# Optimization experiments

Measured on AMD Instinct MI355X. Metric: run time of the kernel, lower is better.

The kernel has to match this reference:

```python
import jax, jax.numpy as jnp
import numpy as np

N, B, L, E = 64, 128, 4096, 16
BN_EPS = 1e-5


def setup_inputs() -> dict:
    key = jax.random.key(0)
    ks = jax.random.split(key, 6)
    feat = jax.random.normal(ks[0], (N, B, L), dtype=jnp.float32)
    # Glorot-ish scaled linear weights
    Wl = jax.random.normal(ks[1], (L, E), dtype=jnp.float32) * (1.0 / np.sqrt(L))
    Wr = jax.random.normal(ks[2], (L, E), dtype=jnp.float32) * (1.0 / np.sqrt(L))
    Wm = jax.random.normal(ks[3], (L, L), dtype=jnp.float32) * (1.0 / np.sqrt(L))
    return {
        "feat": feat,
        "Wl": Wl, "bl": jnp.zeros((E,), jnp.float32),
        "Wr": Wr, "br": jnp.zeros((E,), jnp.float32),
        "Wm": Wm, "bm": jnp.zeros((L,), jnp.float32),
        "gamma": jnp.ones((N * N,), jnp.float32),
        "beta": jnp.zeros((N * N,), jnp.float32),
        "bias": jnp.zeros((L,), jnp.float32),
    }


def reference(feat, Wl, bl, Wr, br, Wm, bm, gamma, beta, bias):
    # feat: (N, B, L) node time series
    # Attention projections (lookup_l / lookup_r): Linear(L -> E)
    att_l = feat @ Wl + bl                      # (N, B, E) on src nodes
    att_r = feat @ Wr + br                      # (N, B, E) on dst nodes

    # Feature extractor: MLP Linear(L, L) + ReLU over the time axis
    out = jax.nn.relu(jnp.einsum('nbl,kl->nbk', feat, Wm) + bm)   # (N, B, L)

    # Edge scores on the complete graph: e[d, s, b] = att_l[src=s] . att_r[dst=d]
    e = jnp.einsum('sbe,dbe->dsb', att_l, att_r)                  # (Nd, Ns, B)

    # BatchNorm1d over N*N edge channels (training-mode batch statistics)
    ef = e.reshape(N * N, B)
    mu = ef.mean(axis=1, keepdims=True)
    var = ef.var(axis=1, keepdims=True)
    ef = gamma[:, None] * (ef - mu) * jax.lax.rsqrt(var + BN_EPS) + beta[:, None]
    e = ef.reshape(N, N, B)

    # edge_softmax: normalize over incoming edges (src axis) per destination node
    w = jax.nn.softmax(e, axis=1)                                  # (Nd, Ns, B)

    # Weighted neighbor aggregation + bias
    rst = jnp.einsum('dsb,sbl->dbl', w, out) + bias                # (N, B, L)
    return rst
```

## Files before the change

### kernel.cpp

```cpp
#include <hip/hip_runtime.h>
#include <stdint.h>
#include <stddef.h>

#define NN 64
#define BB 128
#define LL 4096
#define EE 16

typedef __attribute__((ext_vector_type(4))) float f32x4;
typedef __attribute__((ext_vector_type(2))) float f32x2;
typedef __attribute__((ext_vector_type(8))) short short8;
typedef __attribute__((ext_vector_type(4))) unsigned short u16x4;

__device__ __forceinline__ unsigned short f2bf(float f) {
  union { float f; unsigned u; } v; v.f = f;
  unsigned r = v.u + 0x7FFFu + ((v.u >> 16) & 1u);
  return (unsigned short)(r >> 16);
}
__device__ __forceinline__ float bf2f(unsigned short h) {
  union { unsigned u; float f; } v; v.u = ((unsigned)h) << 16;
  return v.f;
}
__device__ __forceinline__ void gload16(const void* g, void* l) {
  __builtin_amdgcn_global_load_lds((const __attribute__((address_space(1))) void*)g,
                                   (__attribute__((address_space(3))) void*)l,
                                   16, 0, 0);
}

__global__ __launch_bounds__(256) void k_cvt(const float* __restrict__ src,
                                             unsigned short* __restrict__ dst, int n4) {
  int i = blockIdx.x * 256 + threadIdx.x;
  int stride = gridDim.x * 256;
  for (; i < n4; i += stride) {
    f32x4 v = ((const f32x4*)src)[i];
    u16x4 o;
    o[0] = f2bf(v[0]); o[1] = f2bf(v[1]); o[2] = f2bf(v[2]); o[3] = f2bf(v[3]);
    ((u16x4*)dst)[i] = o;
  }
}

__global__ __launch_bounds__(256) void k_att(const float* __restrict__ feat,
    const float* __restrict__ Wl, const float* __restrict__ bl,
    const float* __restrict__ Wr, const float* __restrict__ br,
    unsigned short* __restrict__ feat_bf,
    float* __restrict__ att_l, float* __restrict__ att_r) {
  __shared__ __align__(16) float wlds[128][36];
  __shared__ __align__(16) float flds[8][132];
  __shared__ __align__(16) float red[4][64][4];
  int t = threadIdx.x;
  int rowBase = blockIdx.x * 8;
  int lane = t & 63, wave = t >> 6;
  int row = lane >> 3, eg = lane & 7;
  float acc0 = 0.f, acc1 = 0.f, acc2 = 0.f, acc3 = 0.f;
  for (int kc = 0; kc < 32; ++kc) {
    int k0 = kc * 128;
    __syncthreads();
    for (int i = t; i < 512; i += 256) {
      int kk = i >> 2, ee = (i & 3) * 4;
      *(f32x4*)&wlds[kk][ee]      = *(const f32x4*)&Wl[(size_t)(k0 + kk) * 16 + ee];
      *(f32x4*)&wlds[kk][16 + ee] = *(const f32x4*)&Wr[(size_t)(k0 + kk) * 16 + ee];
    }
    {
      int rr = t >> 5, kk = (t & 31) * 4;
      size_t gi = (size_t)(rowBase + rr) * LL + k0 + kk;
      f32x4 v = *(const f32x4*)&feat[gi];
      *(f32x4*)&flds[rr][kk] = v;
      u16x4 o; o[0] = f2bf(v[0]); o[1] = f2bf(v[1]); o[2] = f2bf(v[2]); o[3] = f2bf(v[3]);
      *(u16x4*)&feat_bf[gi] = o;
    }
    __syncthreads();
    int kb = wave * 32;
    #pragma unroll
    for (int k2 = 0; k2 < 32; ++k2) {
      int k = kb + k2;
      float fv = flds[row][k];
      f32x4 wv = *(const f32x4*)&wlds[k][eg * 4];
      acc0 += fv * wv[0]; acc1 += fv * wv[1]; acc2 += fv * wv[2]; acc3 += fv * wv[3];
    }
  }
  red[wave][lane][0] = acc0; red[wave][lane][1] = acc1;
  red[wave][lane][2] = acc2; red[wave][lane][3] = acc3;
  __syncthreads();
  if (t < 64) {
    f32x4 s = *(f32x4*)&red[0][t][0];
    #pragma unroll
    for (int w2 = 1; w2 < 4; ++w2) {
      f32x4 v = *(f32x4*)&red[w2][t][0];
      s[0] += v[0]; s[1] += v[1]; s[2] += v[2]; s[3] += v[3];
    }
    int r = rowBase + (t >> 3);
    int e0 = (t & 7) * 4;
    #pragma unroll
    for (int q = 0; q < 4; ++q) {
      int e = e0 + q;
      if (e < 16) att_l[(size_t)r * 16 + e]        = s[q] + bl[e];
      else        att_r[(size_t)r * 16 + (e - 16)] = s[q] + br[e - 16];
    }
  }
}

__global__ __launch_bounds__(256) void k_edge(const float* __restrict__ att_l,
    const float* __restrict__ att_r, const float* __restrict__ gamma,
    const float* __restrict__ beta, float* __restrict__ w_t) {
  __shared__ __align__(16) float attr[BB][20];
  __shared__ float el[NN][BB + 1];
  __shared__ float part[NN][4][2];
  __shared__ float sc[NN], sh[NN];
  int d = blockIdx.x, t = threadIdx.x;
  for (int i = t; i < 512; i += 256) {
    int b = i >> 2, e = (i & 3) * 4;
    *(f32x4*)&attr[b][e] = *(const f32x4*)&att_r[((size_t)d * BB + b) * 16 + e];
  }
  __syncthreads();
  for (int v = t; v < NN * BB; v += 256) {
    int s = v >> 7, b = v & 127;
    const float* al = &att_l[((size_t)s * BB + b) * 16];
    float acc = 0.f;
    #pragma unroll
    for (int e4 = 0; e4 < 4; ++e4) {
      f32x4 a = *(const f32x4*)&al[e4 * 4];
      f32x4 r = *(const f32x4*)&attr[b][e4 * 4];
      acc += a[0] * r[0] + a[1] * r[1] + a[2] * r[2] + a[3] * r[3];
    }
    el[s][b] = acc;
  }
  __syncthreads();
  {
    int s = t >> 2, q = t & 3;
    float sum = 0.f, ss = 0.f;
    for (int b = q * 32; b < q * 32 + 32; ++b) { float x = el[s][b]; sum += x; ss += x * x; }
    part[s][q][0] = sum; part[s][q][1] = ss;
  }
  __syncthreads();
  if (t < 64) {
    float sum = 0.f, ss = 0.f;
    #pragma unroll
    for (int q = 0; q < 4; ++q) { sum += part[t][q][0]; ss += part[t][q][1]; }
    float mu = sum * (1.f / 128.f);
    float var = ss * (1.f / 128.f) - mu * mu;
    int c = d * 64 + t;
    float a = gamma[c] * rsqrtf(fmaxf(var, 0.f) + 1e-5f);
    sc[t] = a; sh[t] = beta[c] - mu * a;
  }
  __syncthreads();
  if (t < 128) {
    int b = t;
    float y[64];
    float m = -1e30f;
    #pragma unroll
    for (int s = 0; s < 64; ++s) { y[s] = sc[s] * el[s][b] + sh[s]; m = fmaxf(m, y[s]); }
    float sum = 0.f;
    #pragma unroll
    for (int s = 0; s < 64; ++s) { y[s] = __expf(y[s] - m); sum += y[s]; }
    float inv = 1.f / sum;
    float* wp = &w_t[((size_t)b * 64 + d) * 64];
    #pragma unroll
    for (int s4 = 0; s4 < 16; ++s4) {
      f32x4 o;
      o[0] = y[s4 * 4 + 0] * inv; o[1] = y[s4 * 4 + 1] * inv;
      o[2] = y[s4 * 4 + 2] * inv; o[3] = y[s4 * 4 + 3] * inv;
      *(f32x4*)&wp[s4 * 4] = o;
    }
  }
}

#define LDS_A 0
#define LDS_B 65536
#define BAR   __builtin_amdgcn_s_barrier()
#define LGKM0 asm volatile("s_waitcnt lgkmcnt(0)" ::: "memory")
#define LGKM8 asm volatile("s_waitcnt lgkmcnt(8)" ::: "memory")
#define VM6   asm volatile("s_waitcnt vmcnt(6)" ::: "memory")
#define VM4   asm volatile("s_waitcnt vmcnt(4)" ::: "memory")
#define VM0   asm volatile("s_waitcnt vmcnt(0)" ::: "memory")
#define PRIO1 __builtin_amdgcn_s_setprio(1)
#define PRIO0 __builtin_amdgcn_s_setprio(0)
#define MFMA(a, b, c) __builtin_amdgcn_mfma_f32_16x16x32_bf16((a), (b), (c), 0, 0, 0)
#define STAGE2(g0, g1, ldsoff) do { \
    gload16((g0), lds_raw + (ldsoff) + tid16); \
    gload16((g1), lds_raw + (ldsoff) + 8192 + tid16); } while (0)

__global__ __launch_bounds__(512, 2) void k_gemm8(const unsigned short* __restrict__ A,
    const unsigned short* __restrict__ Bm, const float* __restrict__ bm,
    unsigned short* __restrict__ C) {
  __shared__ __align__(16) char lds_raw[131072];
  const int tid = threadIdx.x;
  const int lane = tid & 63, wave = tid >> 6;
  const int wm = wave >> 2, wn = wave & 3;
  int bid = blockIdx.x;
  int swz = (bid & 7) * 64 + (bid >> 3);
  int tM = swz >> 4, tN = swz & 15;
  const size_t rowBase = (size_t)tM * 256, colBase = (size_t)tN * 256;
  const int tid16 = tid * 16;
  const int o0 = tid16, o1 = tid16 + 8192;
  const int r0s = (o0 & 1023) >> 6, r1s = (o1 & 1023) >> 6;
  const int row0 = (o0 >> 10) * 16 + r0s, row1 = (o1 >> 10) * 16 + r1s;
  const int col0 = (((o0 >> 4) & 3) ^ ((r0s >> 3) << 1)) * 8;
  const int col1 = (((o1 >> 4) & 3) ^ ((r1s >> 3) << 1)) * 8;
  const unsigned short* aR0 = A  + (rowBase + row0) * LL + col0;
  const unsigned short* aR1 = A  + (rowBase + row1) * LL + col1;
  const unsigned short* bR0 = Bm + (colBase + row0) * LL + col0;
  const unsigned short* bR1 = Bm + (colBase + row1) * LL + col1;
  const int rr = lane & 15, gg = lane >> 4;
  const int rdswz = rr * 64 + ((gg ^ ((rr >> 3) << 1)) << 4);
  f32x4 acc[8][4] = {};
  STAGE2(aR0 +  0, aR1 +  0, LDS_A + 0);
  STAGE2(bR0 +  0, bR1 +  0, LDS_B + 0);
  STAGE2(aR0 + 32, aR1 + 32, LDS_A + 16384);
  STAGE2(bR0 + 32, bR1 + 32, LDS_B + 16384);
  VM4;
  STAGE2(aR0 + 64, aR1 + 64, LDS_A + 32768);
  STAGE2(bR0 + 64, bR1 + 64, LDS_B + 32768);
  STAGE2(aR0 + 96, aR1 + 96, LDS_A + 32768 + 16384);
  VM6;
  BAR;
  #pragma unroll 2
  for (int t = 0; t < 64; ++t) {
    const int d = t & 1;
    const char* pA = lds_raw + LDS_A + d * 32768 + wm * 8192 + rdswz;
    const char* pB = lds_raw + LDS_B + d * 32768 + wn * 4096 + rdswz;
    short8 ar[8], bx, by;
    #pragma unroll
    for (int mi = 0; mi < 8; ++mi) ar[mi] = *(const short8*)(pA + mi * 1024);
    bx = *(const short8*)(pB + 0);
    by = *(const short8*)(pB + 1024);
    if (t <= 62) { size_t kc = (size_t)(t + 1) * 64 + 32;
      STAGE2(bR0 + kc, bR1 + kc, LDS_B + ((t + 1) & 1) * 32768 + 16384); }
    LGKM8;
    BAR; LGKM0; PRIO1;
    #pragma unroll
    for (int mi = 0; mi < 8; ++mi) {
      acc[mi][0] = MFMA(ar[mi], bx, acc[mi][0]);
      acc[mi][1] = MFMA(ar[mi], by, acc[mi][1]);
    }
    PRIO0; BAR;
    bx = *(const short8*)(pB + 2048);
    by = *(const short8*)(pB + 3072);
    if (t <= 61) { size_t kc = (size_t)(t + 2) * 64;
      STAGE2(aR0 + kc, aR1 + kc, LDS_A + d * 32768); }
    BAR; LGKM0; PRIO1;
    #pragma unroll
    for (int mi = 0; mi < 8; ++mi) {
      acc[mi][2] = MFMA(ar[mi], bx, acc[mi][2]);
      acc[mi][3] = MFMA(ar[mi], by, acc[mi][3]);
    }
    PRIO0; BAR;
    #pragma unroll
    for (int mi = 0; mi < 8; ++mi) ar[mi] = *(const short8*)(pA + 16384 + mi * 1024);
    bx = *(const short8*)(pB + 16384 + 2048);
    by = *(const short8*)(pB + 16384 + 3072);
    if (t <= 61) { size_t kc = (size_t)(t + 2) * 64;
      STAGE2(bR0 + kc, bR1 + kc, LDS_B + d * 32768); }
    LGKM8;
    BAR; LGKM0; PRIO1;
    #pragma unroll
    for (int mi = 0; mi < 8; ++mi) {
      acc[mi][2] = MFMA(ar[mi], bx, acc[mi][2]);
      acc[mi][3] = MFMA(ar[mi], by, acc[mi][3]);
    }
    PRIO0; BAR;
    bx = *(const short8*)(pB + 16384);
    by = *(const short8*)(pB + 16384 + 1024);
    if (t <= 61) { size_t kc = (size_t)(t + 2) * 64 + 32;
      STAGE2(aR0 + kc, aR1 + kc, LDS_A + d * 32768 + 16384); }
    BAR; LGKM0; PRIO1;
    #pragma unroll
    for (int mi = 0; mi < 8; ++mi) {
      acc[mi][0] = MFMA(ar[mi], bx, acc[mi][0]);
      acc[mi][1] = MFMA(ar[mi], by, acc[mi][1]);
    }
    PRIO0;
    if (t < 62) { VM6; } else { VM0; }
    BAR;
  }
  const int co = lane & 15, ro4 = (lane >> 4) * 4;
  #pragma unroll
  for (int mig = 0; mig < 8; ++mig) {
    size_t r0 = rowBase + (size_t)wm * 128 + mig * 16 + ro4;
    #pragma unroll
    for (int nj = 0; nj < 4; ++nj) {
      size_t c = colBase + (size_t)wn * 64 + nj * 16 + co;
      float bc = bm[c];
      #pragma unroll
      for (int j = 0; j < 4; ++j) {
        float v = acc[mig][nj][j] + bc;
        v = fmaxf(v, 0.f);
        C[(r0 + j) * LL + c] = f2bf(v);
      }
    }
  }
}

__global__ __launch_bounds__(256) void k_agg2(const float* __restrict__ w_t,
    const unsigned short* __restrict__ outb, const float* __restrict__ bias,
    float* __restrict__ rst) {
  int b = blockIdx.y;
  int t = threadIdx.x;
  int l0 = blockIdx.x * 512 + t * 2;
  float oA[64], oB[64];
  #pragma unroll
  for (int s = 0; s < 64; ++s) {
    unsigned u = *(const unsigned*)&outb[((size_t)s * BB + b) * LL + l0];
    oA[s] = bf2f((unsigned short)(u & 0xFFFF));
    oB[s] = bf2f((unsigned short)(u >> 16));
  }
  const float* wb = w_t + (size_t)b * 4096;
  float bs0 = bias[l0], bs1 = bias[l0 + 1];
  #pragma unroll 2
  for (int d = 0; d < 64; ++d) {
    const float* wr = wb + d * 64;
    float a0 = 0.f, a1 = 0.f;
    #pragma unroll
    for (int q = 0; q < 16; ++q) {
      f32x4 wq = *(const f32x4*)&wr[q * 4];
      #pragma unroll
      for (int j = 0; j < 4; ++j) {
        float wv = wq[j];
        a0 += wv * oA[q * 4 + j];
        a1 += wv * oB[q * 4 + j];
      }
    }
    f32x2 o; o[0] = a0 + bs0; o[1] = a1 + bs1;
    *(f32x2*)&rst[((size_t)d * BB + b) * LL + l0] = o;
  }
}

extern "C" void kernel_launch(void* const* d_in, const int* in_sizes, int n_in,
                              void* d_out, int out_size, void* d_ws, size_t ws_size,
                              hipStream_t stream) {
  (void)in_sizes; (void)n_in; (void)out_size; (void)ws_size;
  const float* feat  = (const float*)d_in[0];
  const float* Wl    = (const float*)d_in[1];
  const float* bl    = (const float*)d_in[2];
  const float* Wr    = (const float*)d_in[3];
  const float* br    = (const float*)d_in[4];
  const float* Wm    = (const float*)d_in[5];
  const float* bm    = (const float*)d_in[6];
  const float* gamma = (const float*)d_in[7];
  const float* beta  = (const float*)d_in[8];
  const float* bias  = (const float*)d_in[9];
  char* ws = (char*)d_ws;
  unsigned short* feat_bf = (unsigned short*)(ws);
  unsigned short* wm_bf   = (unsigned short*)(ws + 67108864ull);
  unsigned short* out_bf  = (unsigned short*)(ws + 100663296ull);
  float* att_l = (float*)(ws + 167772160ull);
  float* att_r = (float*)(ws + 168296448ull);
  float* w_t   = (float*)(ws + 168820736ull);
  float* rst = (float*)d_out;

  k_cvt<<<dim3(2048), dim3(256), 0, stream>>>(Wm, wm_bf, (LL * LL) / 4);
  k_att<<<dim3(1024), dim3(256), 0, stream>>>(feat, Wl, bl, Wr, br, feat_bf, att_l, att_r);
  k_edge<<<dim3(64), dim3(256), 0, stream>>>(att_l, att_r, gamma, beta, w_t);
  k_gemm8<<<dim3(512), dim3(512), 0, stream>>>(feat_bf, wm_bf, bm, out_bf);
  k_agg2<<<dim3(8, 128), dim3(256), 0, stream>>>(w_t, out_bf, bias, rst);
}
```

Baseline: 447.9 us.

## Compute attention projections with bf16 MFMA split-K and drop explicit LDS waits

Replaces the fp32 LDS-based attention projection kernel with a separate feat-to-bf16 conversion plus an MFMA split-K kernel over a transposed bf16 copy of Wl/Wr. The four partial sums are reduced inside the edge kernel together with the biases. The main GEMM also drops its manual lgkmcnt waits and reorders the LDS fragment loads, leaving wait placement to the compiler. This trades fp32 precision in the attention scores for bf16, adds an extra pass that reads feat for the conversion, and makes the edge kernel do more global reads.

```diff
diff --git a/kernel.cpp b/kernel.cpp
--- a/kernel.cpp
+++ b/kernel.cpp
@@ -27,101 +27,110 @@
                                    16, 0, 0);
 }
 
-__global__ __launch_bounds__(256) void k_cvt(const float* __restrict__ src,
-                                             unsigned short* __restrict__ dst, int n4) {
+__global__ __launch_bounds__(256) void k_cvtw(const float* __restrict__ Wm,
+    const float* __restrict__ Wl, const float* __restrict__ Wr,
+    unsigned short* __restrict__ wm_bf, unsigned short* __restrict__ wt_bf) {
+  int bid = blockIdx.x;
+  if (bid < 2048) {
+    int i = bid * 256 + threadIdx.x;
+    for (; i < (LL * LL / 4); i += 2048 * 256) {
+      f32x4 v = ((const f32x4*)Wm)[i];
+      u16x4 o;
+      o[0] = f2bf(v[0]); o[1] = f2bf(v[1]); o[2] = f2bf(v[2]); o[3] = f2bf(v[3]);
+      ((u16x4*)wm_bf)[i] = o;
+    }
+  } else {
+    int u = (bid - 2048) * 256 + threadIdx.x;
+    int e = u >> 6;
+    int kb = (u & 63) * 64;
+    const float* src = (e < 16) ? (Wl + e) : (Wr + (e - 16));
+    for (int k = kb; k < kb + 64; ++k)
+      wt_bf[(size_t)e * LL + k] = f2bf(src[(size_t)k * 16]);
+  }
+}
+
+__global__ __launch_bounds__(256) void k_cvtf(const float* __restrict__ feat,
+                                              unsigned short* __restrict__ feat_bf) {
   int i = blockIdx.x * 256 + threadIdx.x;
-  int stride = gridDim.x * 256;
-  for (; i < n4; i += stride) {
-    f32x4 v = ((const f32x4*)src)[i];
+  const int n4 = NN * BB * LL / 4;
+  for (; i < n4; i += 2048 * 256) {
+    f32x4 v = ((const f32x4*)feat)[i];
     u16x4 o;
     o[0] = f2bf(v[0]); o[1] = f2bf(v[1]); o[2] = f2bf(v[2]); o[3] = f2bf(v[3]);
-    ((u16x4*)dst)[i] = o;
-  }
-}
-
-__global__ __launch_bounds__(256) void k_att(const float* __restrict__ feat,
-    const float* __restrict__ Wl, const float* __restrict__ bl,
-    const float* __restrict__ Wr, const float* __restrict__ br,
-    unsigned short* __restrict__ feat_bf,
-    float* __restrict__ att_l, float* __restrict__ att_r) {
-  __shared__ __align__(16) float wlds[128][36];
-  __shared__ __align__(16) float flds[8][132];
-  __shared__ __align__(16) float red[4][64][4];
-  int t = threadIdx.x;
-  int rowBase = blockIdx.x * 8;
-  int lane = t & 63, wave = t >> 6;
-  int row = lane >> 3, eg = lane & 7;
-  float acc0 = 0.f, acc1 = 0.f, acc2 = 0.f, acc3 = 0.f;
-  for (int kc = 0; kc < 32; ++kc) {
-    int k0 = kc * 128;
-    __syncthreads();
-    for (int i = t; i < 512; i += 256) {
-      int kk = i >> 2, ee = (i & 3) * 4;
-      *(f32x4*)&wlds[kk][ee]      = *(const f32x4*)&Wl[(size_t)(k0 + kk) * 16 + ee];
-      *(f32x4*)&wlds[kk][16 + ee] = *(const f32x4*)&Wr[(size_t)(k0 + kk) * 16 + ee];
-    }
-    {
-      int rr = t >> 5, kk = (t & 31) * 4;
-      size_t gi = (size_t)(rowBase + rr) * LL + k0 + kk;
-      f32x4 v = *(const f32x4*)&feat[gi];
-      *(f32x4*)&flds[rr][kk] = v;
-      u16x4 o; o[0] = f2bf(v[0]); o[1] = f2bf(v[1]); o[2] = f2bf(v[2]); o[3] = f2bf(v[3]);
-      *(u16x4*)&feat_bf[gi] = o;
-    }
-    __syncthreads();
-    int kb = wave * 32;
-    #pragma unroll
-    for (int k2 = 0; k2 < 32; ++k2) {
-      int k = kb + k2;
-      float fv = flds[row][k];
-      f32x4 wv = *(const f32x4*)&wlds[k][eg * 4];
-      acc0 += fv * wv[0]; acc1 += fv * wv[1]; acc2 += fv * wv[2]; acc3 += fv * wv[3];
-    }
-  }
-  red[wave][lane][0] = acc0; red[wave][lane][1] = acc1;
-  red[wave][lane][2] = acc2; red[wave][lane][3] = acc3;
-  __syncthreads();
-  if (t < 64) {
-    f32x4 s = *(f32x4*)&red[0][t][0];
-    #pragma unroll
-    for (int w2 = 1; w2 < 4; ++w2) {
-      f32x4 v = *(f32x4*)&red[w2][t][0];
-      s[0] += v[0]; s[1] += v[1]; s[2] += v[2]; s[3] += v[3];
-    }
-    int r = rowBase + (t >> 3);
-    int e0 = (t & 7) * 4;
-    #pragma unroll
-    for (int q = 0; q < 4; ++q) {
-      int e = e0 + q;
-      if (e < 16) att_l[(size_t)r * 16 + e]        = s[q] + bl[e];
-      else        att_r[(size_t)r * 16 + (e - 16)] = s[q] + br[e - 16];
-    }
-  }
-}
-
-__global__ __launch_bounds__(256) void k_edge(const float* __restrict__ att_l,
-    const float* __restrict__ att_r, const float* __restrict__ gamma,
-    const float* __restrict__ beta, float* __restrict__ w_t) {
+    ((u16x4*)feat_bf)[i] = o;
+  }
+}
+
+#define MFMA(a, b, c) __builtin_amdgcn_mfma_f32_16x16x32_bf16((a), (b), (c), 0, 0, 0)
+
+__global__ __launch_bounds__(256) void k_attm(const unsigned short* __restrict__ feat_bf,
+    const unsigned short* __restrict__ wt_bf, float* __restrict__ attP) {
+  const int t = threadIdx.x, lane = t & 63, w = t >> 6;
+  const int rowTile = blockIdx.x;
+  const int kc = blockIdx.y;
+  const int grow = rowTile * 64 + w * 16 + (lane & 15);
+  const int kbase = kc * 1024 + (lane >> 4) * 8;
+  const unsigned short* aP  = feat_bf + (size_t)grow * LL + kbase;
+  const unsigned short* b0P = wt_bf + (size_t)(lane & 15) * LL + kbase;
+  const unsigned short* b1P = wt_bf + (size_t)(16 + (lane & 15)) * LL + kbase;
+  f32x4 acc0 = {}, acc1 = {};
+  #pragma unroll 4
+  for (int ks = 0; ks < 32; ++ks) {
+    short8 av = *(const short8*)(aP + ks * 32);
+    short8 b0 = *(const short8*)(b0P + ks * 32);
+    short8 b1 = *(const short8*)(b1P + ks * 32);
+    acc0 = MFMA(av, b0, acc0);
+    acc1 = MFMA(av, b1, acc1);
+  }
+  const int orow = rowTile * 64 + w * 16 + (lane >> 4) * 4;
+  const int col = lane & 15;
+  float* P = attP + (size_t)kc * (8192 * 32);
+  #pragma unroll
+  for (int j = 0; j < 4; ++j) {
+    P[(size_t)(orow + j) * 32 + col]      = acc0[j];
+    P[(size_t)(orow + j) * 32 + 16 + col] = acc1[j];
+  }
+}
+
+__global__ __launch_bounds__(256) void k_edge(const float* __restrict__ attP,
+    const float* __restrict__ bl, const float* __restrict__ br,
+    const float* __restrict__ gamma, const float* __restrict__ beta,
+    float* __restrict__ w_t) {
   __shared__ __align__(16) float attr[BB][20];
   __shared__ float el[NN][BB + 1];
   __shared__ float part[NN][4][2];
   __shared__ float sc[NN], sh[NN];
   int d = blockIdx.x, t = threadIdx.x;
-  for (int i = t; i < 512; i += 256) {
-    int b = i >> 2, e = (i & 3) * 4;
-    *(f32x4*)&attr[b][e] = *(const f32x4*)&att_r[((size_t)d * BB + b) * 16 + e];
-  }
+  for (int i = t; i < 2048; i += 256) {
+    int b = i >> 4, e = i & 15;
+    float v2 = br[e];
+    #pragma unroll
+    for (int c = 0; c < 4; ++c)
+      v2 += attP[(size_t)c * (8192 * 32) + ((size_t)d * 128 + b) * 32 + 16 + e];
+    attr[b][e] = v2;
+  }
+  float blv[16];
+  #pragma unroll
+  for (int e = 0; e < 16; ++e) blv[e] = bl[e];
   __syncthreads();
   for (int v = t; v < NN * BB; v += 256) {
     int s = v >> 7, b = v & 127;
-    const float* al = &att_l[((size_t)s * BB + b) * 16];
+    float al[16];
+    #pragma unroll
+    for (int e = 0; e < 16; ++e) al[e] = blv[e];
+    #pragma unroll
+    for (int c = 0; c < 4; ++c) {
+      const f32x4* p = (const f32x4*)&attP[(size_t)c * (8192 * 32) + ((size_t)s * 128 + b) * 32];
+      #pragma unroll
+      for (int q = 0; q < 4; ++q) {
+        f32x4 x = p[q];
+        al[q * 4 + 0] += x[0]; al[q * 4 + 1] += x[1];
+        al[q * 4 + 2] += x[2]; al[q * 4 + 3] += x[3];
+      }
+    }
     float acc = 0.f;
     #pragma unroll
-    for (int e4 = 0; e4 < 4; ++e4) {
-      f32x4 a = *(const f32x4*)&al[e4 * 4];
-      f32x4 r = *(const f32x4*)&attr[b][e4 * 4];
-      acc += a[0] * r[0] + a[1] * r[1] + a[2] * r[2] + a[3] * r[3];
-    }
+    for (int e = 0; e < 16; ++e) acc += al[e] * attr[b][e];
     el[s][b] = acc;
   }
   __syncthreads();
@@ -167,14 +176,11 @@
 #define LDS_A 0
 #define LDS_B 65536
 #define BAR   __builtin_amdgcn_s_barrier()
-#define LGKM0 asm volatile("s_waitcnt lgkmcnt(0)" ::: "memory")
-#define LGKM8 asm volatile("s_waitcnt lgkmcnt(8)" ::: "memory")
 #define VM6   asm volatile("s_waitcnt vmcnt(6)" ::: "memory")
 #define VM4   asm volatile("s_waitcnt vmcnt(4)" ::: "memory")
 #define VM0   asm volatile("s_waitcnt vmcnt(0)" ::: "memory")
 #define PRIO1 __builtin_amdgcn_s_setprio(1)
 #define PRIO0 __builtin_amdgcn_s_setprio(0)
-#define MFMA(a, b, c) __builtin_amdgcn_mfma_f32_16x16x32_bf16((a), (b), (c), 0, 0, 0)
 #define STAGE2(g0, g1, ldsoff) do { \
     gload16((g0), lds_raw + (ldsoff) + tid16); \
     gload16((g1), lds_raw + (ldsoff) + 8192 + tid16); } while (0)
@@ -219,14 +225,13 @@
     const char* pA = lds_raw + LDS_A + d * 32768 + wm * 8192 + rdswz;
     const char* pB = lds_raw + LDS_B + d * 32768 + wn * 4096 + rdswz;
     short8 ar[8], bx, by;
-    #pragma unroll
-    for (int mi = 0; mi < 8; ++mi) ar[mi] = *(const short8*)(pA + mi * 1024);
     bx = *(const short8*)(pB + 0);
     by = *(const short8*)(pB + 1024);
+    #pragma unroll
+    for (int mi = 0; mi < 8; ++mi) ar[mi] = *(const short8*)(pA + mi * 1024);
     if (t <= 62) { size_t kc = (size_t)(t + 1) * 64 + 32;
       STAGE2(bR0 + kc, bR1 + kc, LDS_B + ((t + 1) & 1) * 32768 + 16384); }
-    LGKM8;
-    BAR; LGKM0; PRIO1;
+    BAR; PRIO1;
     #pragma unroll
     for (int mi = 0; mi < 8; ++mi) {
       acc[mi][0] = MFMA(ar[mi], bx, acc[mi][0]);
@@ -237,21 +242,20 @@
     by = *(const short8*)(pB + 3072);
     if (t <= 61) { size_t kc = (size_t)(t + 2) * 64;
       STAGE2(aR0 + kc, aR1 + kc, LDS_A + d * 32768); }
-    BAR; LGKM0; PRIO1;
+    BAR; PRIO1;
     #pragma unroll
     for (int mi = 0; mi < 8; ++mi) {
       acc[mi][2] = MFMA(ar[mi], bx, acc[mi][2]);
       acc[mi][3] = MFMA(ar[mi], by, acc[mi][3]);
     }
     PRIO0; BAR;
-    #pragma unroll
-    for (int mi = 0; mi < 8; ++mi) ar[mi] = *(const short8*)(pA + 16384 + mi * 1024);
     bx = *(const short8*)(pB + 16384 + 2048);
     by = *(const short8*)(pB + 16384 + 3072);
+    #pragma unroll
+    for (int mi = 0; mi < 8; ++mi) ar[mi] = *(const short8*)(pA + 16384 + mi * 1024);
     if (t <= 61) { size_t kc = (size_t)(t + 2) * 64;
       STAGE2(bR0 + kc, bR1 + kc, LDS_B + d * 32768); }
-    LGKM8;
-    BAR; LGKM0; PRIO1;
+    BAR; PRIO1;
     #pragma unroll
     for (int mi = 0; mi < 8; ++mi) {
       acc[mi][2] = MFMA(ar[mi], bx, acc[mi][2]);
@@ -262,7 +266,7 @@
     by = *(const short8*)(pB + 16384 + 1024);
     if (t <= 61) { size_t kc = (size_t)(t + 2) * 64 + 32;
       STAGE2(aR0 + kc, aR1 + kc, LDS_A + d * 32768 + 16384); }
-    BAR; LGKM0; PRIO1;
+    BAR; PRIO1;
     #pragma unroll
     for (int mi = 0; mi < 8; ++mi) {
       acc[mi][0] = MFMA(ar[mi], bx, acc[mi][0]);
@@ -342,14 +346,15 @@
   unsigned short* feat_bf = (unsigned short*)(ws);
   unsigned short* wm_bf   = (unsigned short*)(ws + 67108864ull);
   unsigned short* out_bf  = (unsigned short*)(ws + 100663296ull);
-  float* att_l = (float*)(ws + 167772160ull);
-  float* att_r = (float*)(ws + 168296448ull);
-  float* w_t   = (float*)(ws + 168820736ull);
+  float* attP  = (float*)(ws + 167772160ull);
+  float* w_t   = (float*)(ws + 171966464ull);
+  unsigned short* wt_bf = (unsigned short*)(ws + 174063616ull);
   float* rst = (float*)d_out;
 
-  k_cvt<<<dim3(2048), dim3(256), 0, stream>>>(Wm, wm_bf, (LL * LL) / 4);
-  k_att<<<dim3(1024), dim3(256), 0, stream>>>(feat, Wl, bl, Wr, br, feat_bf, att_l, att_r);
-  k_edge<<<dim3(64), dim3(256), 0, stream>>>(att_l, att_r, gamma, beta, w_t);
+  k_cvtw<<<dim3(2056), dim3(256), 0, stream>>>(Wm, Wl, Wr, wm_bf, wt_bf);
+  k_cvtf<<<dim3(2048), dim3(256), 0, stream>>>(feat, feat_bf);
+  k_attm<<<dim3(128, 4), dim3(256), 0, stream>>>(feat_bf, wt_bf, attP);
+  k_edge<<<dim3(64), dim3(256), 0, stream>>>(attP, bl, br, gamma, beta, w_t);
   k_gemm8<<<dim3(512), dim3(512), 0, stream>>>(feat_bf, wm_bf, bm, out_bf);
   k_agg2<<<dim3(8, 128), dim3(256), 0, stream>>>(w_t, out_bf, bias, rst);
 }
```

New measurement: 478.1 us. 1.07x slower.
